# Kernel optimization log

Hardware: AMD Instinct MI355X
Metric: run time of the kernel (lower is better)

Reference implementation:

```python
import jax, jax.numpy as jnp
import numpy as np

NUM_ITERS = 15
EPSILON = 0.05
MESH_ITERS = 3


def _cost_proj(x, W1, b1, W2, b2):
    # Linear -> ReLU -> Linear
    h = jax.nn.relu(x @ W1 + b1)
    return h @ W2 + b2


def setup_inputs() -> dict:
    key = jax.random.key(0)
    ks = jax.random.split(key, 4)
    B, K, M, D = 8192, 32, 32, 256
    s = 1.0 / np.sqrt(D)
    return {
        "slots_q": jax.random.normal(ks[0], (B, K, D), dtype=jnp.float32),
        "slots_r": jax.random.normal(ks[1], (B, M, D), dtype=jnp.float32),
        "W1": (jax.random.normal(ks[2], (D, D), dtype=jnp.float32) * s),
        "b1": jnp.zeros((D,), dtype=jnp.float32),
        "W2": (jax.random.normal(ks[3], (D, D), dtype=jnp.float32) * s),
        "b2": jnp.zeros((D,), dtype=jnp.float32),
    }


def reference(slots_q, slots_r, W1, b1, W2, b2):
    q = _cost_proj(slots_q, W1, b1, W2, b2)  # [B,K,D]
    r = _cost_proj(slots_r, W1, b1, W2, b2)  # [B,M,D]
    # torch.cdist p=2: pairwise euclidean distance
    sq = (jnp.sum(q * q, -1)[:, :, None]
          + jnp.sum(r * r, -1)[:, None, :]
          - 2.0 * jnp.einsum('bkd,bmd->bkm', q, r))
    C = jnp.sqrt(jnp.clip(sq, 0.0))  # [B,K,M]
    B, K, M = C.shape
    log_K = -C / EPSILON
    log_a = jnp.zeros((B, K, 1), dtype=C.dtype)
    log_b = jnp.zeros((B, 1, M), dtype=C.dtype)
    for _ in range(NUM_ITERS):
        log_a = -jax.nn.logsumexp(log_K + log_b, axis=2, keepdims=True)
        log_b = -jax.nn.logsumexp(log_K + log_a, axis=1, keepdims=True)
    T = jnp.exp(log_K + log_a + log_b)
    for _ in range(MESH_ITERS):
        T = T ** 2
        T = T / (jnp.sum(T, axis=-1, keepdims=True) + 1e-8)
        T = T / (jnp.sum(T, axis=-2, keepdims=True) + 1e-8)
    cost = jnp.sum(T * C, axis=(-1, -2))  # [B]
    similarity = jax.nn.sigmoid(-cost)
    return similarity, T, C, cost
```

## Files before the change

kernel.cpp:

```cpp
#include <hip/hip_runtime.h>
#include <hip/hip_bf16.h>


typedef unsigned short u16;
typedef short short8 __attribute__((ext_vector_type(8)));
typedef float f32x4  __attribute__((ext_vector_type(4)));

#define MFMA(a, b, c) __builtin_amdgcn_mfma_f32_16x16x32_bf16((a), (b), (c), 0, 0, 0)

static __device__ __forceinline__ u16 f2bf(float f) {
  __hip_bfloat16 h = __float2bfloat16(f);
  return __builtin_bit_cast(u16, h);
}
static __device__ __forceinline__ float bf2f(u16 h) {
  return __uint_as_float(((unsigned)h) << 16);
}

__global__ __launch_bounds__(256) void prep_w(const float* __restrict__ W1,
                                              const float* __restrict__ W2,
                                              u16* __restrict__ ws) {
  int id = blockIdx.x * 256 + threadIdx.x;
  int mat = id >> 16;
  int e = id & 65535;
  int k = e >> 8, n = e & 255;
  float wv = (mat ? W2 : W1)[e];
  int ki = k >> 5, kl = k & 31;
  int g = kl >> 3, j = kl & 7;
  int lane = g * 16 + (n & 15);
  int ctg = n >> 4;
  ws[mat * 65536 + ((((ki * 16 + ctg) * 64 + lane) << 3) | j)] = f2bf(wv);
}

struct __align__(16) SMemA {
  u16 F[16384];
  float nrm[64];
};

static __device__ __forceinline__ void gemm_frag(const u16* __restrict__ Af,
                                                 const u16* __restrict__ wf,
                                                 int w, int lane, f32x4 acc[4][2]) {
#pragma unroll
  for (int rt = 0; rt < 4; ++rt) {
    acc[rt][0] = f32x4{0.f, 0.f, 0.f, 0.f};
    acc[rt][1] = f32x4{0.f, 0.f, 0.f, 0.f};
  }
  __builtin_amdgcn_s_setprio(1);
#pragma unroll
  for (int ki = 0; ki < 8; ++ki) {
    const u16* bp = wf + (((ki * 16 + 2 * w) * 64 + lane) << 3);
    short8 b0 = *reinterpret_cast<const short8*>(bp);
    short8 b1 = *reinterpret_cast<const short8*>(bp + 512);
    short8 a[4];
#pragma unroll
    for (int rt = 0; rt < 4; ++rt)
      a[rt] = *reinterpret_cast<const short8*>(Af + (((ki * 4 + rt) * 64 + lane) << 3));
#pragma unroll
    for (int rt = 0; rt < 4; ++rt) {
      acc[rt][0] = MFMA(a[rt], b0, acc[rt][0]);
      acc[rt][1] = MFMA(a[rt], b1, acc[rt][1]);
    }
  }
  __builtin_amdgcn_s_setprio(0);
}

__global__ __launch_bounds__(512, 8) void gemm_cdist(
    const float* __restrict__ slots_q, const float* __restrict__ slots_r,
    const float* __restrict__ b1, const float* __restrict__ b2,
    const u16* __restrict__ ws, float* __restrict__ CO) {
  __shared__ SMemA sm;
  const int tid = threadIdx.x, b = blockIdx.x;
  const int w = tid >> 6, lane = tid & 63, g = lane >> 4, ln = lane & 15;

  {
    const float* srcq = slots_q + (size_t)b * 8192;
    const float* srcr = slots_r + (size_t)b * 8192;
#pragma unroll
    for (int ii = 0; ii < 4; ++ii) {
      int s = tid + ii * 512;
      int ki = s >> 8, rt = (s >> 6) & 3, sg = (s >> 4) & 3, sln = s & 15;
      int row = rt * 16 + sln;
      const float* src = (row < 32) ? (srcq + row * 256) : (srcr + (row - 32) * 256);
      int k0 = ki * 32 + sg * 8;
      f32x4 v0 = __builtin_nontemporal_load(
          reinterpret_cast<const f32x4*>(src + k0));
      f32x4 v1 = __builtin_nontemporal_load(
          reinterpret_cast<const f32x4*>(src + k0 + 4));
      short8 o;
      o[0] = (short)f2bf(v0[0]); o[1] = (short)f2bf(v0[1]);
      o[2] = (short)f2bf(v0[2]); o[3] = (short)f2bf(v0[3]);
      o[4] = (short)f2bf(v1[0]); o[5] = (short)f2bf(v1[1]);
      o[6] = (short)f2bf(v1[2]); o[7] = (short)f2bf(v1[3]);
      *reinterpret_cast<short8*>(&sm.F[s << 3]) = o;
    }
  }
  float bv1a = b1[32 * w + ln], bv1b = b1[32 * w + 16 + ln];
  float bv2a = b2[32 * w + ln], bv2b = b2[32 * w + 16 + ln];
  __syncthreads();

  f32x4 acc[4][2];
  gemm_frag(sm.F, ws, w, lane, acc);
  __syncthreads();
#pragma unroll
  for (int ct = 0; ct < 2; ++ct) {
    float bv = ct ? bv1b : bv1a;
#pragma unroll
    for (int rt = 0; rt < 4; ++rt)
#pragma unroll
      for (int ri = 0; ri < 4; ++ri) {
        int lane2 = (2 * ct + (ln >> 3)) * 16 + 4 * g + ri;
        sm.F[(((w * 4 + rt) * 64 + lane2) << 3) | (ln & 7)] =
            f2bf(fmaxf(acc[rt][ct][ri] + bv, 0.0f));
      }
  }
  __syncthreads();

  gemm_frag(sm.F, ws + 65536, w, lane, acc);
  __syncthreads();
#pragma unroll
  for (int ct = 0; ct < 2; ++ct) {
    float bv = ct ? bv2b : bv2a;
#pragma unroll
    for (int rt = 0; rt < 4; ++rt)
#pragma unroll
      for (int ri = 0; ri < 4; ++ri) {
        int lane2 = (2 * ct + (ln >> 3)) * 16 + 4 * g + ri;
        sm.F[(((w * 4 + rt) * 64 + lane2) << 3) | (ln & 7)] =
            f2bf(acc[rt][ct][ri] + bv);
      }
  }
  __syncthreads();

  f32x4 dacc = f32x4{0.f, 0.f, 0.f, 0.f};
  if (w < 4) {
    const int mt = w >> 1, nt = w & 1;
    __builtin_amdgcn_s_setprio(1);
#pragma unroll
    for (int ki = 0; ki < 8; ++ki) {
      short8 aq = *reinterpret_cast<const short8*>(
          &sm.F[(((ki * 4 + mt) * 64 + lane) << 3)]);
      short8 br = *reinterpret_cast<const short8*>(
          &sm.F[(((ki * 4 + 2 + nt) * 64 + lane) << 3)]);
      dacc = MFMA(aq, br, dacc);
    }
    __builtin_amdgcn_s_setprio(0);
  } else {
    const int t = w - 4;
    float s = 0.f;
#pragma unroll
    for (int ki = 0; ki < 8; ++ki) {
      short8 v = *reinterpret_cast<const short8*>(
          &sm.F[(((ki * 4 + t) * 64 + lane) << 3)]);
#pragma unroll
      for (int i = 0; i < 8; ++i) {
        float f = bf2f((u16)v[i]);
        s = fmaf(f, f, s);
      }
    }
    s += __shfl_xor(s, 16);
    s += __shfl_xor(s, 32);
    if (lane < 16) sm.nrm[t * 16 + lane] = s;
  }
  __syncthreads();

  if (w < 4) {
    const int mt = w >> 1, nt = w & 1;
    float* Cp = CO + (size_t)b * 1024;
#pragma unroll
    for (int ri = 0; ri < 4; ++ri) {
      int k = mt * 16 + 4 * g + ri;
      int m = nt * 16 + ln;
      float sq = sm.nrm[k] + sm.nrm[32 + m] - 2.0f * dacc[ri];
      Cp[k * 32 + m] = sqrtf(fmaxf(sq, 0.0f));
    }
  }
}

__global__ __launch_bounds__(256, 4) void sinkhorn_mesh(
    const float* __restrict__ CO, float* __restrict__ simO,
    float* __restrict__ TO, float* __restrict__ costO, int Bn) {
  __shared__ float Wl[4][32 * 33];
  __shared__ float ABl[4][64];
  const int wv = threadIdx.x >> 6, lane = threadIdx.x & 63;
  const int p = blockIdx.x * 4 + wv;
  if (p >= Bn) return;
  const int h = lane >> 5, q = lane & 31;
  float* Wm = Wl[wv];
  float* LA = ABl[wv];
  float* LB = ABl[wv] + 32;
  const float* Cp = CO + (size_t)p * 1024;

  float lkr[16], lkc[16];
#pragma unroll
  for (int jj = 0; jj < 4; ++jj) {
    f32x4 v = *reinterpret_cast<const f32x4*>(Cp + q * 32 + h * 16 + jj * 4);
    int base = q * 33 + h * 16 + jj * 4;
    Wm[base + 0] = v[0]; Wm[base + 1] = v[1]; Wm[base + 2] = v[2]; Wm[base + 3] = v[3];
    lkr[jj * 4 + 0] = -20.f * v[0]; lkr[jj * 4 + 1] = -20.f * v[1];
    lkr[jj * 4 + 2] = -20.f * v[2]; lkr[jj * 4 + 3] = -20.f * v[3];
  }
  LB[q] = 0.0f;
  __builtin_amdgcn_wave_barrier();
#pragma unroll
  for (int j = 0; j < 16; ++j) lkc[j] = -20.f * Wm[(h * 16 + j) * 33 + q];

  for (int it = 0; it < 15; ++it) {
    float v[16], mx, s;
#pragma unroll
    for (int j = 0; j < 16; ++j) v[j] = lkr[j] + LB[h * 16 + j];
    mx = v[0];
#pragma unroll
    for (int j = 1; j < 16; ++j) mx = fmaxf(mx, v[j]);
    mx = fmaxf(mx, __shfl_xor(mx, 32));
    s = 0.f;
#pragma unroll
    for (int j = 0; j < 16; ++j) s += __expf(v[j] - mx);
    s += __shfl_xor(s, 32);
    LA[q] = -(mx + __logf(s));
    __builtin_amdgcn_wave_barrier();
#pragma unroll
    for (int j = 0; j < 16; ++j) v[j] = lkc[j] + LA[h * 16 + j];
    mx = v[0];
#pragma unroll
    for (int j = 1; j < 16; ++j) mx = fmaxf(mx, v[j]);
    mx = fmaxf(mx, __shfl_xor(mx, 32));
    s = 0.f;
#pragma unroll
    for (int j = 0; j < 16; ++j) s += __expf(v[j] - mx);
    s += __shfl_xor(s, 32);
    LB[q] = -(mx + __logf(s));
    __builtin_amdgcn_wave_barrier();
  }

  float t[16];
  {
    float la = LA[q];
#pragma unroll
    for (int j = 0; j < 16; ++j) t[j] = __expf(lkr[j] + la + LB[h * 16 + j]);
  }

  for (int mi = 0; mi < 3; ++mi) {
    float s = 0.f;
#pragma unroll
    for (int j = 0; j < 16; ++j) { t[j] *= t[j]; s += t[j]; }
    s += __shfl_xor(s, 32);
    float inv = 1.0f / (s + 1e-8f);
#pragma unroll
    for (int j = 0; j < 16; ++j) Wm[q * 33 + h * 16 + j] = t[j] * inv;
    __builtin_amdgcn_wave_barrier();
#pragma unroll
    for (int j = 0; j < 16; ++j) t[j] = Wm[(h * 16 + j) * 33 + q];
    s = 0.f;
#pragma unroll
    for (int j = 0; j < 16; ++j) s += t[j];
    s += __shfl_xor(s, 32);
    inv = 1.0f / (s + 1e-8f);
#pragma unroll
    for (int j = 0; j < 16; ++j) Wm[(h * 16 + j) * 33 + q] = t[j] * inv;
    __builtin_amdgcn_wave_barrier();
#pragma unroll
    for (int j = 0; j < 16; ++j) t[j] = Wm[q * 33 + h * 16 + j];
  }

  float pp = 0.f;
#pragma unroll
  for (int j = 0; j < 16; ++j) pp = fmaf(t[j], -0.05f * lkr[j], pp);
  pp += __shfl_xor(pp, 1); pp += __shfl_xor(pp, 2); pp += __shfl_xor(pp, 4);
  pp += __shfl_xor(pp, 8); pp += __shfl_xor(pp, 16); pp += __shfl_xor(pp, 32);
  if (lane == 0) {
    costO[p] = pp;
    simO[p] = 1.0f / (1.0f + __expf(pp));
  }
#pragma unroll
  for (int jj = 0; jj < 4; ++jj) {
    f32x4 o;
    o[0] = t[jj * 4 + 0]; o[1] = t[jj * 4 + 1];
    o[2] = t[jj * 4 + 2]; o[3] = t[jj * 4 + 3];
    __builtin_nontemporal_store(
        o, reinterpret_cast<f32x4*>(TO + (size_t)p * 1024 + q * 32 + h * 16 + jj * 4));
  }
}

extern "C" void kernel_launch(void* const* d_in, const int* in_sizes, int n_in,
                              void* d_out, int out_size, void* d_ws, size_t ws_size,
                              hipStream_t stream) {
  const float* slots_q = (const float*)d_in[0];
  const float* slots_r = (const float*)d_in[1];
  const float* W1 = (const float*)d_in[2];
  const float* b1 = (const float*)d_in[3];
  const float* W2 = (const float*)d_in[4];
  const float* b2 = (const float*)d_in[5];
  float* out = (float*)d_out;

  const int Bn = in_sizes[0] / 8192;
  u16* ws = (u16*)d_ws;

  prep_w<<<dim3(512), dim3(256), 0, stream>>>(W1, W2, ws);

  float* simO = out;
  float* TO = out + Bn;
  float* CO = TO + (size_t)Bn * 1024;
  float* costO = CO + (size_t)Bn * 1024;

  gemm_cdist<<<dim3(Bn), dim3(512), 0, stream>>>(slots_q, slots_r, b1, b2, ws, CO);
  sinkhorn_mesh<<<dim3((Bn + 3) / 4), dim3(256), 0, stream>>>(CO, simO, TO, costO, Bn);
}
```

Baseline: 263.8 us.

## Process two batch items per block with 128-row GEMM tiles to reuse weights

Each block of the projection+cdist kernel now handles two batch elements (128 rows) instead of one, and each wave computes a 64x64 output tile (4x4 MFMA fragments) instead of 64x32. This halves the number of weight-fragment loads from global memory per row and improves the MFMA-to-load ratio, and all 8 waves now do both the norm and the cross-distance MFMA rather than splitting the work. In exchange, LDS use doubles to about 64KB and accumulators double, so occupancy drops (launch bounds 8 to 4 blocks), and the grid halves.

```diff
diff --git a/kernel.cpp b/kernel.cpp
--- a/kernel.cpp
+++ b/kernel.cpp
@@ -31,60 +31,74 @@
   ws[mat * 65536 + ((((ki * 16 + ctg) * 64 + lane) << 3) | j)] = f2bf(wv);
 }
 
-struct __align__(16) SMemA {
-  u16 F[16384];
-  float nrm[64];
+struct __align__(16) SMemA2 {
+  u16 F[32768];
+  float nrm[128];
 };
 
-static __device__ __forceinline__ void gemm_frag(const u16* __restrict__ Af,
-                                                 const u16* __restrict__ wf,
-                                                 int w, int lane, f32x4 acc[4][2]) {
-#pragma unroll
-  for (int rt = 0; rt < 4; ++rt) {
-    acc[rt][0] = f32x4{0.f, 0.f, 0.f, 0.f};
-    acc[rt][1] = f32x4{0.f, 0.f, 0.f, 0.f};
-  }
+static __device__ __forceinline__ void gemm_frag2(const u16* __restrict__ Af,
+                                                  const u16* __restrict__ wf,
+                                                  int rh, int cq, int lane,
+                                                  f32x4 acc[4][4]) {
+#pragma unroll
+  for (int rt = 0; rt < 4; ++rt)
+#pragma unroll
+    for (int ct = 0; ct < 4; ++ct) acc[rt][ct] = f32x4{0.f, 0.f, 0.f, 0.f};
   __builtin_amdgcn_s_setprio(1);
 #pragma unroll
   for (int ki = 0; ki < 8; ++ki) {
-    const u16* bp = wf + (((ki * 16 + 2 * w) * 64 + lane) << 3);
-    short8 b0 = *reinterpret_cast<const short8*>(bp);
-    short8 b1 = *reinterpret_cast<const short8*>(bp + 512);
     short8 a[4];
 #pragma unroll
     for (int rt = 0; rt < 4; ++rt)
-      a[rt] = *reinterpret_cast<const short8*>(Af + (((ki * 4 + rt) * 64 + lane) << 3));
-#pragma unroll
-    for (int rt = 0; rt < 4; ++rt) {
-      acc[rt][0] = MFMA(a[rt], b0, acc[rt][0]);
-      acc[rt][1] = MFMA(a[rt], b1, acc[rt][1]);
+      a[rt] = *reinterpret_cast<const short8*>(
+          Af + (((ki * 8 + 4 * rh + rt) * 64 + lane) << 3));
+    const u16* bp = wf + (((ki * 16 + 4 * cq) * 64 + lane) << 3);
+    {
+      short8 bx = *reinterpret_cast<const short8*>(bp);
+      short8 by = *reinterpret_cast<const short8*>(bp + 512);
+#pragma unroll
+      for (int rt = 0; rt < 4; ++rt) {
+        acc[rt][0] = MFMA(a[rt], bx, acc[rt][0]);
+        acc[rt][1] = MFMA(a[rt], by, acc[rt][1]);
+      }
+    }
+    {
+      short8 bx = *reinterpret_cast<const short8*>(bp + 1024);
+      short8 by = *reinterpret_cast<const short8*>(bp + 1536);
+#pragma unroll
+      for (int rt = 0; rt < 4; ++rt) {
+        acc[rt][2] = MFMA(a[rt], bx, acc[rt][2]);
+        acc[rt][3] = MFMA(a[rt], by, acc[rt][3]);
+      }
     }
   }
   __builtin_amdgcn_s_setprio(0);
 }
 
-__global__ __launch_bounds__(512, 8) void gemm_cdist(
+__global__ __launch_bounds__(512, 4) void gemm_cdist2(
     const float* __restrict__ slots_q, const float* __restrict__ slots_r,
     const float* __restrict__ b1, const float* __restrict__ b2,
-    const u16* __restrict__ ws, float* __restrict__ CO) {
-  __shared__ SMemA sm;
-  const int tid = threadIdx.x, b = blockIdx.x;
+    const u16* __restrict__ ws, float* __restrict__ CO, int Bn) {
+  __shared__ SMemA2 sm;
+  const int tid = threadIdx.x;
   const int w = tid >> 6, lane = tid & 63, g = lane >> 4, ln = lane & 15;
+  const int rh = w & 1, cq = w >> 1;
+  const int pb = blockIdx.x * 2;
 
   {
-    const float* srcq = slots_q + (size_t)b * 8192;
-    const float* srcr = slots_r + (size_t)b * 8192;
-#pragma unroll
-    for (int ii = 0; ii < 4; ++ii) {
+#pragma unroll
+    for (int ii = 0; ii < 8; ++ii) {
       int s = tid + ii * 512;
-      int ki = s >> 8, rt = (s >> 6) & 3, sg = (s >> 4) & 3, sln = s & 15;
+      int sln = s & 15, sg = (s >> 4) & 3, rt = (s >> 6) & 7, ki = s >> 9;
       int row = rt * 16 + sln;
-      const float* src = (row < 32) ? (srcq + row * 256) : (srcr + (row - 32) * 256);
+      int P = row >> 6, rl = row & 63;
+      int pidx = (pb + P < Bn) ? (pb + P) : (Bn - 1);
+      size_t base = (size_t)pidx * 8192;
+      const float* src = (rl < 32) ? (slots_q + base + rl * 256)
+                                   : (slots_r + base + (rl - 32) * 256);
       int k0 = ki * 32 + sg * 8;
-      f32x4 v0 = __builtin_nontemporal_load(
-          reinterpret_cast<const f32x4*>(src + k0));
-      f32x4 v1 = __builtin_nontemporal_load(
-          reinterpret_cast<const f32x4*>(src + k0 + 4));
+      f32x4 v0 = __builtin_nontemporal_load(reinterpret_cast<const f32x4*>(src + k0));
+      f32x4 v1 = __builtin_nontemporal_load(reinterpret_cast<const f32x4*>(src + k0 + 4));
       short8 o;
       o[0] = (short)f2bf(v0[0]); o[1] = (short)f2bf(v0[1]);
       o[2] = (short)f2bf(v0[2]); o[3] = (short)f2bf(v0[3]);
@@ -93,63 +107,59 @@
       *reinterpret_cast<short8*>(&sm.F[s << 3]) = o;
     }
   }
-  float bv1a = b1[32 * w + ln], bv1b = b1[32 * w + 16 + ln];
-  float bv2a = b2[32 * w + ln], bv2b = b2[32 * w + 16 + ln];
-  __syncthreads();
-
-  f32x4 acc[4][2];
-  gemm_frag(sm.F, ws, w, lane, acc);
-  __syncthreads();
-#pragma unroll
-  for (int ct = 0; ct < 2; ++ct) {
-    float bv = ct ? bv1b : bv1a;
-#pragma unroll
-    for (int rt = 0; rt < 4; ++rt)
+  __syncthreads();
+
+  f32x4 acc[4][4];
+  gemm_frag2(sm.F, ws, rh, cq, lane, acc);
+  float bv0 = b1[64 * cq + ln],      bv1 = b1[64 * cq + 16 + ln];
+  float bv2 = b1[64 * cq + 32 + ln], bv3 = b1[64 * cq + 48 + ln];
+  __syncthreads();
+#pragma unroll
+  for (int ct = 0; ct < 4; ++ct) {
+    float bv = (ct == 0) ? bv0 : (ct == 1) ? bv1 : (ct == 2) ? bv2 : bv3;
+    int ki2 = 2 * cq + (ct >> 1);
+    int g2 = 2 * (ct & 1) + (ln >> 3);
+#pragma unroll
+    for (int rt = 0; rt < 4; ++rt) {
+      int rtg = 4 * rh + rt;
 #pragma unroll
       for (int ri = 0; ri < 4; ++ri) {
-        int lane2 = (2 * ct + (ln >> 3)) * 16 + 4 * g + ri;
-        sm.F[(((w * 4 + rt) * 64 + lane2) << 3) | (ln & 7)] =
+        int lane2 = g2 * 16 + 4 * g + ri;
+        sm.F[(((ki2 * 8 + rtg) * 64 + lane2) << 3) | (ln & 7)] =
             f2bf(fmaxf(acc[rt][ct][ri] + bv, 0.0f));
       }
-  }
-  __syncthreads();
-
-  gemm_frag(sm.F, ws + 65536, w, lane, acc);
-  __syncthreads();
-#pragma unroll
-  for (int ct = 0; ct < 2; ++ct) {
-    float bv = ct ? bv2b : bv2a;
-#pragma unroll
-    for (int rt = 0; rt < 4; ++rt)
+    }
+  }
+  __syncthreads();
+
+  gemm_frag2(sm.F, ws + 65536, rh, cq, lane, acc);
+  float cv0 = b2[64 * cq + ln],      cv1 = b2[64 * cq + 16 + ln];
+  float cv2 = b2[64 * cq + 32 + ln], cv3 = b2[64 * cq + 48 + ln];
+  __syncthreads();
+#pragma unroll
+  for (int ct = 0; ct < 4; ++ct) {
+    float bv = (ct == 0) ? cv0 : (ct == 1) ? cv1 : (ct == 2) ? cv2 : cv3;
+    int ki2 = 2 * cq + (ct >> 1);
+    int g2 = 2 * (ct & 1) + (ln >> 3);
+#pragma unroll
+    for (int rt = 0; rt < 4; ++rt) {
+      int rtg = 4 * rh + rt;
 #pragma unroll
       for (int ri = 0; ri < 4; ++ri) {
-        int lane2 = (2 * ct + (ln >> 3)) * 16 + 4 * g + ri;
-        sm.F[(((w * 4 + rt) * 64 + lane2) << 3) | (ln & 7)] =
+        int lane2 = g2 * 16 + 4 * g + ri;
+        sm.F[(((ki2 * 8 + rtg) * 64 + lane2) << 3) | (ln & 7)] =
             f2bf(acc[rt][ct][ri] + bv);
       }
-  }
-  __syncthreads();
-
-  f32x4 dacc = f32x4{0.f, 0.f, 0.f, 0.f};
-  if (w < 4) {
-    const int mt = w >> 1, nt = w & 1;
-    __builtin_amdgcn_s_setprio(1);
-#pragma unroll
-    for (int ki = 0; ki < 8; ++ki) {
-      short8 aq = *reinterpret_cast<const short8*>(
-          &sm.F[(((ki * 4 + mt) * 64 + lane) << 3)]);
-      short8 br = *reinterpret_cast<const short8*>(
-          &sm.F[(((ki * 4 + 2 + nt) * 64 + lane) << 3)]);
-      dacc = MFMA(aq, br, dacc);
-    }
-    __builtin_amdgcn_s_setprio(0);
-  } else {
-    const int t = w - 4;
+    }
+  }
+  __syncthreads();
+
+  {
     float s = 0.f;
 #pragma unroll
     for (int ki = 0; ki < 8; ++ki) {
       short8 v = *reinterpret_cast<const short8*>(
-          &sm.F[(((ki * 4 + t) * 64 + lane) << 3)]);
+          &sm.F[(((ki * 8 + w) * 64 + lane) << 3)]);
 #pragma unroll
       for (int i = 0; i < 8; ++i) {
         float f = bf2f((u16)v[i]);
@@ -158,18 +168,29 @@
     }
     s += __shfl_xor(s, 16);
     s += __shfl_xor(s, 32);
-    if (lane < 16) sm.nrm[t * 16 + lane] = s;
-  }
-  __syncthreads();
-
-  if (w < 4) {
-    const int mt = w >> 1, nt = w & 1;
-    float* Cp = CO + (size_t)b * 1024;
+    if (lane < 16) sm.nrm[w * 16 + lane] = s;
+  }
+  const int P = w >> 2, mt = (w >> 1) & 1, nt = w & 1;
+  f32x4 dacc = f32x4{0.f, 0.f, 0.f, 0.f};
+  __builtin_amdgcn_s_setprio(1);
+#pragma unroll
+  for (int ki = 0; ki < 8; ++ki) {
+    short8 aq = *reinterpret_cast<const short8*>(
+        &sm.F[(((ki * 8 + 4 * P + mt) * 64 + lane) << 3)]);
+    short8 br = *reinterpret_cast<const short8*>(
+        &sm.F[(((ki * 8 + 4 * P + 2 + nt) * 64 + lane) << 3)]);
+    dacc = MFMA(aq, br, dacc);
+  }
+  __builtin_amdgcn_s_setprio(0);
+  __syncthreads();
+
+  if (pb + P < Bn) {
+    float* Cp = CO + (size_t)(pb + P) * 1024;
 #pragma unroll
     for (int ri = 0; ri < 4; ++ri) {
       int k = mt * 16 + 4 * g + ri;
       int m = nt * 16 + ln;
-      float sq = sm.nrm[k] + sm.nrm[32 + m] - 2.0f * dacc[ri];
+      float sq = sm.nrm[64 * P + k] + sm.nrm[64 * P + 32 + m] - 2.0f * dacc[ri];
       Cp[k * 32 + m] = sqrtf(fmaxf(sq, 0.0f));
     }
   }
@@ -301,6 +322,7 @@
   float* CO = TO + (size_t)Bn * 1024;
   float* costO = CO + (size_t)Bn * 1024;
 
-  gemm_cdist<<<dim3(Bn), dim3(512), 0, stream>>>(slots_q, slots_r, b1, b2, ws, CO);
+  gemm_cdist2<<<dim3((Bn + 1) / 2), dim3(512), 0, stream>>>(slots_q, slots_r,
+                                                            b1, b2, ws, CO, Bn);
   sinkhorn_mesh<<<dim3((Bn + 3) / 4), dim3(256), 0, stream>>>(CO, simO, TO, costO, Bn);
 }
```

Result: no change. 263.1 us (-0.3%).
